# Kernel tuning notes

Hardware: AMD Instinct MI355X
Metric: run time of the kernel (lower is better)

Reference implementation:

```python
import jax, jax.numpy as jnp
import numpy as np


def setup_inputs() -> dict:
    key = jax.random.key(0)
    k1, k2, k3, k4, k5 = jax.random.split(key, 5)
    B, C, H, W = 8, 32, 64, 64
    inp = jax.random.normal(k1, (B, C, H, W), dtype=jnp.float32)
    # expected positions lie inside the image grid
    exPx = jax.random.uniform(k2, (B, H, W), dtype=jnp.float32) * (W - 1)
    exPy = jax.random.uniform(k3, (B, H, W), dtype=jnp.float32) * (H - 1)
    # positive Gaussian widths in roughly [1, 3]
    sigmax = jax.random.uniform(k4, (B, H, W), dtype=jnp.float32) * 2.0 + 1.0
    sigmay = jax.random.uniform(k5, (B, H, W), dtype=jnp.float32) * 2.0 + 1.0
    return {"input": inp, "exPx": exPx, "exPy": exPy,
            "sigmax": sigmax, "sigmay": sigmay}


def reference(input, exPx, exPy, sigmax, sigmay):
    """Gaussian-weighted spatial swap/warp (soft gather).

    For each output pixel (i, j):
      out[b,c,i,j] = sum_{u,v} G(u; exPy[b,i,j], sigmay[b,i,j])
                              * G(v; exPx[b,i,j], sigmax[b,i,j])
                              * input[b,c,u,v]  /  Z[b,i,j]
    where G is an unnormalized Gaussian and Z is the total weight mass.
    The 2D Gaussian weight is separable, so we contract rows then cols.
    """
    B, C, H, W = input.shape
    u = jnp.arange(H, dtype=input.dtype)  # source row coords (y)
    v = jnp.arange(W, dtype=input.dtype)  # source col coords (x)
    # wy: [B,H,W,H] weight over source rows u for each output pixel (i,j)
    wy = jnp.exp(-0.5 * ((u[None, None, None, :] - exPy[..., None]) / sigmay[..., None]) ** 2)
    # wx: [B,H,W,W] weight over source cols v
    wx = jnp.exp(-0.5 * ((v[None, None, None, :] - exPx[..., None]) / sigmax[..., None]) ** 2)
    # normalization mass per output pixel
    Z = wy.sum(-1) * wx.sum(-1) + jnp.asarray(1e-8, input.dtype)  # [B,H,W]
    # contract over source rows u -> [B,C,H,W,W]
    t = jnp.einsum('biju,bcuv->bcijv', wy, input)
    # contract over source cols v -> [B,C,H,W]
    out = jnp.einsum('bcijv,bijv->bcij', t, wx)
    return out / Z[:, None]
```

## Files before the change

kernel.cpp:

```cpp
#include <hip/hip_runtime.h>


#define BB 8
#define CC 32
#define HH 64
#define WW 64

typedef __attribute__((ext_vector_type(8))) short short8;
typedef __attribute__((ext_vector_type(4))) float f32x4;
typedef unsigned int uint;

__device__ __forceinline__ uint rn_bf16(float f) {
    uint u = __float_as_uint(f);
    return (u + 0x7FFFu + ((u >> 16) & 1u)) >> 16;
}

__device__ __forceinline__ void split_pair(float f0, float f1, uint& hi, uint& lo) {
    const uint u0 = __float_as_uint(f0), u1 = __float_as_uint(f1);
    hi = (u0 >> 16) | (u1 & 0xFFFF0000u);
    const float l0 = f0 - __uint_as_float(u0 & 0xFFFF0000u);
    const float l1 = f1 - __uint_as_float(u1 & 0xFFFF0000u);
    lo = (__float_as_uint(l0) >> 16) | (__float_as_uint(l1) & 0xFFFF0000u);
}

#define WYS_OFF   0
#define WXH_OFF   16640
#define SUM_OFF   25856
#define INVZ_OFF  27904
#define LDS_BYTES 28160
#define RED_OFF   0

__global__ __launch_bounds__(256, 4)
void swap_fused_kernel(const float* __restrict__ inp,
                       const float* __restrict__ exPx, const float* __restrict__ exPy,
                       const float* __restrict__ sigmax, const float* __restrict__ sigmay,
                       float* __restrict__ out)
{
    __shared__ __align__(16) char lds[LDS_BYTES];
    const int t    = threadIdx.x;
    const int lane = t & 63;
    const int w    = t >> 6;
    const int q    = (t >> 4) & 3;
    const int ln   = t & 15;
    const int bid   = blockIdx.x;
    const int b     = bid & 7;
    const int r     = bid >> 3;
    const int chalf = r & 1;
    const int i     = r >> 1;
    const int bi    = b * 64 + i;

    float* WYS = (float*)(lds + WYS_OFF);

    {
        const int p = lane;
        const int g = w;
        const int pixBase = bi * 64 + p;
        const float ey = exPy[pixBase], ex = exPx[pixBase];
        const float isy = 1.0f / sigmay[pixBase], isx = 1.0f / sigmax[pixBase];
        float sy = 0.0f, sx = 0.0f;
        #pragma unroll
        for (int k = 0; k < 16; ++k) {
            const int u = g * 16 + k;
            const float dy = ((float)u - ey) * isy;
            const float wy = __expf(-0.5f * dy * dy);
            WYS[u * 65 + p] = wy;
            sy += wy;
        }
        uint* WXH = (uint*)(lds + WXH_OFF);
        #pragma unroll
        for (int j = 0; j < 8; ++j) {
            const int v0 = g * 16 + 2 * j;
            const float dx0 = ((float)v0       - ex) * isx;
            const float dx1 = ((float)(v0 + 1) - ex) * isx;
            const float wx0 = __expf(-0.5f * dx0 * dx0);
            const float wx1 = __expf(-0.5f * dx1 * dx1);
            sx += wx0 + wx1;
            WXH[p * 36 + g * 8 + j] = rn_bf16(wx0) | (rn_bf16(wx1) << 16);
        }
        float* SUMY = (float*)(lds + SUM_OFF);
        float* SUMX = SUMY + 256;
        SUMY[g * 64 + p] = sy;
        SUMX[g * 64 + p] = sx;
    }
    __syncthreads();
    float* INVZ = (float*)(lds + INVZ_OFF);
    if (t < 64) {
        float* SUMY = (float*)(lds + SUM_OFF);
        float* SUMX = SUMY + 256;
        const float sy = SUMY[t] + SUMY[64 + t] + SUMY[128 + t] + SUMY[192 + t];
        const float sx = SUMX[t] + SUMX[64 + t] + SUMX[128 + t] + SUMX[192 + t];
        INVZ[t] = 1.0f / (sy * sx + 1e-8f);
    }
    __syncthreads();

    short8 bh[4][2];
    #pragma unroll
    for (int nt = 0; nt < 4; ++nt)
        #pragma unroll
        for (int ks = 0; ks < 2; ++ks)
            bh[nt][ks] = *(const short8*)(lds + WXH_OFF + (nt * 16 + ln) * 144 + ks * 64 + q * 16);
    float wyz[4][4];
    #pragma unroll
    for (int nt = 0; nt < 4; ++nt) {
        const float iz = INVZ[nt * 16 + ln];
        #pragma unroll
        for (int rr = 0; rr < 4; ++rr)
            wyz[nt][rr] = WYS[(w * 16 + q * 4 + rr) * 65 + nt * 16 + ln] * iz;
    }
    __syncthreads();

    const int cbase = b * CC + chalf * 16;
    float* RED = (float*)(lds + RED_OFF);
    const float* xrow = inp + (size_t)cbase * 4096 + (w * 16 + ln) * 64 + q * 8;

    #pragma unroll 2
    for (int c = 0; c < 16; ++c) {
        const float4* src = (const float4*)(xrow + (size_t)c * 4096);
        const float4 x0 = src[0];
        const float4 x1 = src[1];
        const float4 x2 = src[8];
        const float4 x3 = src[9];

        union { uint u[4]; short8 s; } Ah0, Al0, Ah1, Al1;
        split_pair(x0.x, x0.y, Ah0.u[0], Al0.u[0]);
        split_pair(x0.z, x0.w, Ah0.u[1], Al0.u[1]);
        split_pair(x1.x, x1.y, Ah0.u[2], Al0.u[2]);
        split_pair(x1.z, x1.w, Ah0.u[3], Al0.u[3]);
        split_pair(x2.x, x2.y, Ah1.u[0], Al1.u[0]);
        split_pair(x2.z, x2.w, Ah1.u[1], Al1.u[1]);
        split_pair(x3.x, x3.y, Ah1.u[2], Al1.u[2]);
        split_pair(x3.z, x3.w, Ah1.u[3], Al1.u[3]);

        f32x4 acc[4];
        #pragma unroll
        for (int nt = 0; nt < 4; ++nt) acc[nt] = (f32x4){0.f, 0.f, 0.f, 0.f};
        #pragma unroll
        for (int nt = 0; nt < 4; ++nt) {
            acc[nt] = __builtin_amdgcn_mfma_f32_16x16x32_bf16(Ah0.s, bh[nt][0], acc[nt], 0, 0, 0);
            acc[nt] = __builtin_amdgcn_mfma_f32_16x16x32_bf16(Al0.s, bh[nt][0], acc[nt], 0, 0, 0);
            acc[nt] = __builtin_amdgcn_mfma_f32_16x16x32_bf16(Ah1.s, bh[nt][1], acc[nt], 0, 0, 0);
            acc[nt] = __builtin_amdgcn_mfma_f32_16x16x32_bf16(Al1.s, bh[nt][1], acc[nt], 0, 0, 0);
        }
        #pragma unroll
        for (int nt = 0; nt < 4; ++nt) {
            float ps = acc[nt][0] * wyz[nt][0] + acc[nt][1] * wyz[nt][1]
                     + acc[nt][2] * wyz[nt][2] + acc[nt][3] * wyz[nt][3];
            ps += __shfl_xor(ps, 16, 64);
            ps += __shfl_xor(ps, 32, 64);
            if (q == 0) RED[c * 256 + w * 64 + nt * 16 + ln] = ps;
        }
    }
    __syncthreads();

    {
        const int kk = t >> 6, p = t & 63;
        #pragma unroll
        for (int g = 0; g < 4; ++g) {
            const int c = g * 4 + kk;
            const float* Rk = RED + c * 256;
            const float o = Rk[p] + Rk[64 + p] + Rk[128 + p] + Rk[192 + p];
            out[(size_t)(cbase + c) * (HH * WW) + i * 64 + p] = o;
        }
    }
}

extern "C" void kernel_launch(void* const* d_in, const int* in_sizes, int n_in,
                              void* d_out, int out_size, void* d_ws, size_t ws_size,
                              hipStream_t stream) {
    const float* inp    = (const float*)d_in[0];
    const float* exPx   = (const float*)d_in[1];
    const float* exPy   = (const float*)d_in[2];
    const float* sigmax = (const float*)d_in[3];
    const float* sigmay = (const float*)d_in[4];
    float* out = (float*)d_out;

    hipLaunchKernelGGL(swap_fused_kernel, dim3(BB * HH * 2), dim3(256), 0, stream,
                       inp, exPx, exPy, sigmax, sigmay, out);
}
```

Before: 93.08 us.

## Preconvert input to bf16 in workspace and drop hi/lo split MFMAs

Adds a pre-pass kernel that rounds the float32 input to packed bf16 in the workspace buffer. The main kernel then loads half the bytes per row and issues only the high-part MFMAs, halving the matrix-core work and removing the per-iteration split arithmetic. The cost is an extra launch and a full read/write pass over the input, plus lower accuracy because the low-part correction term is dropped. The old fused kernel remains as a fallback when the workspace is too small.

After: 82.25 us. 1.13x faster.

```diff
diff --git a/kernel.cpp b/kernel.cpp
--- a/kernel.cpp
+++ b/kernel.cpp
@@ -15,12 +15,14 @@
     return (u + 0x7FFFu + ((u >> 16) & 1u)) >> 16;
 }
 
-__device__ __forceinline__ void split_pair(float f0, float f1, uint& hi, uint& lo) {
-    const uint u0 = __float_as_uint(f0), u1 = __float_as_uint(f1);
-    hi = (u0 >> 16) | (u1 & 0xFFFF0000u);
-    const float l0 = f0 - __uint_as_float(u0 & 0xFFFF0000u);
-    const float l1 = f1 - __uint_as_float(u1 & 0xFFFF0000u);
-    lo = (__float_as_uint(l0) >> 16) | (__float_as_uint(l1) & 0xFFFF0000u);
+__global__ void preconvert_kernel(const float* __restrict__ x, uint* __restrict__ hi)
+{
+    const int n = BB * CC * HH * WW / 2;
+    int idx = blockIdx.x * blockDim.x + threadIdx.x;
+    for (; idx < n; idx += gridDim.x * blockDim.x) {
+        const float2 d = ((const float2*)x)[idx];
+        hi[idx] = rn_bf16(d.x) | (rn_bf16(d.y) << 16);
+    }
 }
 
 #define WYS_OFF   0
@@ -31,10 +33,10 @@
 #define RED_OFF   0
 
 __global__ __launch_bounds__(256, 4)
-void swap_fused_kernel(const float* __restrict__ inp,
-                       const float* __restrict__ exPx, const float* __restrict__ exPy,
-                       const float* __restrict__ sigmax, const float* __restrict__ sigmay,
-                       float* __restrict__ out)
+void swap_mfma_kernel(const uint* __restrict__ xhi,
+                      const float* __restrict__ exPx, const float* __restrict__ exPy,
+                      const float* __restrict__ sigmax, const float* __restrict__ sigmay,
+                      float* __restrict__ out)
 {
     __shared__ __align__(16) char lds[LDS_BYTES];
     const int t    = threadIdx.x;
@@ -111,16 +113,129 @@
 
     const int cbase = b * CC + chalf * 16;
     float* RED = (float*)(lds + RED_OFF);
+    const uint* xrow = xhi + (size_t)cbase * 2048 + (w * 16 + ln) * 32 + q * 4;
+
+    #pragma unroll 4
+    for (int c = 0; c < 16; ++c) {
+        const uint4* src = (const uint4*)(xrow + (size_t)c * 2048);
+        union { uint4 v; short8 s; } A0, A1;
+        A0.v = src[0];
+        A1.v = src[4];
+
+        f32x4 acc[4];
+        #pragma unroll
+        for (int nt = 0; nt < 4; ++nt) acc[nt] = (f32x4){0.f, 0.f, 0.f, 0.f};
+        #pragma unroll
+        for (int nt = 0; nt < 4; ++nt) {
+            acc[nt] = __builtin_amdgcn_mfma_f32_16x16x32_bf16(A0.s, bh[nt][0], acc[nt], 0, 0, 0);
+            acc[nt] = __builtin_amdgcn_mfma_f32_16x16x32_bf16(A1.s, bh[nt][1], acc[nt], 0, 0, 0);
+        }
+        #pragma unroll
+        for (int nt = 0; nt < 4; ++nt) {
+            float ps = acc[nt][0] * wyz[nt][0] + acc[nt][1] * wyz[nt][1]
+                     + acc[nt][2] * wyz[nt][2] + acc[nt][3] * wyz[nt][3];
+            ps += __shfl_xor(ps, 16, 64);
+            ps += __shfl_xor(ps, 32, 64);
+            if (q == 0) RED[c * 256 + w * 64 + nt * 16 + ln] = ps;
+        }
+    }
+    __syncthreads();
+
+    {
+        const int kk = t >> 6, p = t & 63;
+        #pragma unroll
+        for (int g = 0; g < 4; ++g) {
+            const int c = g * 4 + kk;
+            const float* Rk = RED + c * 256;
+            const float o = Rk[p] + Rk[64 + p] + Rk[128 + p] + Rk[192 + p];
+            out[(size_t)(cbase + c) * (HH * WW) + i * 64 + p] = o;
+        }
+    }
+}
+
+__device__ __forceinline__ void split_pair(float f0, float f1, uint& hi, uint& lo) {
+    const uint u0 = __float_as_uint(f0), u1 = __float_as_uint(f1);
+    hi = (u0 >> 16) | (u1 & 0xFFFF0000u);
+    const float l0 = f0 - __uint_as_float(u0 & 0xFFFF0000u);
+    const float l1 = f1 - __uint_as_float(u1 & 0xFFFF0000u);
+    lo = (__float_as_uint(l0) >> 16) | (__float_as_uint(l1) & 0xFFFF0000u);
+}
+
+__global__ __launch_bounds__(256, 4)
+void swap_fused_kernel(const float* __restrict__ inp,
+                       const float* __restrict__ exPx, const float* __restrict__ exPy,
+                       const float* __restrict__ sigmax, const float* __restrict__ sigmay,
+                       float* __restrict__ out)
+{
+    __shared__ __align__(16) char lds[LDS_BYTES];
+    const int t = threadIdx.x;
+    const int lane = t & 63, w = t >> 6, q = (t >> 4) & 3, ln = t & 15;
+    const int bid = blockIdx.x;
+    const int b = bid & 7, r = bid >> 3;
+    const int chalf = r & 1, i = r >> 1;
+    const int bi = b * 64 + i;
+
+    float* WYS = (float*)(lds + WYS_OFF);
+    {
+        const int p = lane, g = w;
+        const int pixBase = bi * 64 + p;
+        const float ey = exPy[pixBase], ex = exPx[pixBase];
+        const float isy = 1.0f / sigmay[pixBase], isx = 1.0f / sigmax[pixBase];
+        float sy = 0.0f, sx = 0.0f;
+        #pragma unroll
+        for (int k = 0; k < 16; ++k) {
+            const int u = g * 16 + k;
+            const float dy = ((float)u - ey) * isy;
+            const float wy = __expf(-0.5f * dy * dy);
+            WYS[u * 65 + p] = wy; sy += wy;
+        }
+        uint* WXH = (uint*)(lds + WXH_OFF);
+        #pragma unroll
+        for (int j = 0; j < 8; ++j) {
+            const int v0 = g * 16 + 2 * j;
+            const float dx0 = ((float)v0 - ex) * isx;
+            const float dx1 = ((float)(v0 + 1) - ex) * isx;
+            const float wx0 = __expf(-0.5f * dx0 * dx0);
+            const float wx1 = __expf(-0.5f * dx1 * dx1);
+            sx += wx0 + wx1;
+            WXH[p * 36 + g * 8 + j] = rn_bf16(wx0) | (rn_bf16(wx1) << 16);
+        }
+        float* SUMY = (float*)(lds + SUM_OFF);
+        float* SUMX = SUMY + 256;
+        SUMY[g * 64 + p] = sy; SUMX[g * 64 + p] = sx;
+    }
+    __syncthreads();
+    float* INVZ = (float*)(lds + INVZ_OFF);
+    if (t < 64) {
+        float* SUMY = (float*)(lds + SUM_OFF);
+        float* SUMX = SUMY + 256;
+        const float sy = SUMY[t] + SUMY[64 + t] + SUMY[128 + t] + SUMY[192 + t];
+        const float sx = SUMX[t] + SUMX[64 + t] + SUMX[128 + t] + SUMX[192 + t];
+        INVZ[t] = 1.0f / (sy * sx + 1e-8f);
+    }
+    __syncthreads();
+    short8 bh[4][2];
+    #pragma unroll
+    for (int nt = 0; nt < 4; ++nt)
+        #pragma unroll
+        for (int ks = 0; ks < 2; ++ks)
+            bh[nt][ks] = *(const short8*)(lds + WXH_OFF + (nt * 16 + ln) * 144 + ks * 64 + q * 16);
+    float wyz[4][4];
+    #pragma unroll
+    for (int nt = 0; nt < 4; ++nt) {
+        const float iz = INVZ[nt * 16 + ln];
+        #pragma unroll
+        for (int rr = 0; rr < 4; ++rr)
+            wyz[nt][rr] = WYS[(w * 16 + q * 4 + rr) * 65 + nt * 16 + ln] * iz;
+    }
+    __syncthreads();
+    const int cbase = b * CC + chalf * 16;
+    float* RED = (float*)(lds + RED_OFF);
     const float* xrow = inp + (size_t)cbase * 4096 + (w * 16 + ln) * 64 + q * 8;
-
     #pragma unroll 2
     for (int c = 0; c < 16; ++c) {
         const float4* src = (const float4*)(xrow + (size_t)c * 4096);
-        const float4 x0 = src[0];
-        const float4 x1 = src[1];
-        const float4 x2 = src[8];
-        const float4 x3 = src[9];
-
+        const float4 x0 = src[0], x1 = src[1], x2 = src[8], x3 = src[9];
         union { uint u[4]; short8 s; } Ah0, Al0, Ah1, Al1;
         split_pair(x0.x, x0.y, Ah0.u[0], Al0.u[0]);
         split_pair(x0.z, x0.w, Ah0.u[1], Al0.u[1]);
@@ -130,7 +245,6 @@
         split_pair(x2.z, x2.w, Ah1.u[1], Al1.u[1]);
         split_pair(x3.x, x3.y, Ah1.u[2], Al1.u[2]);
         split_pair(x3.z, x3.w, Ah1.u[3], Al1.u[3]);
-
         f32x4 acc[4];
         #pragma unroll
         for (int nt = 0; nt < 4; ++nt) acc[nt] = (f32x4){0.f, 0.f, 0.f, 0.f};
@@ -151,7 +265,6 @@
         }
     }
     __syncthreads();
-
     {
         const int kk = t >> 6, p = t & 63;
         #pragma unroll
@@ -174,6 +287,14 @@
     const float* sigmay = (const float*)d_in[4];
     float* out = (float*)d_out;
 
-    hipLaunchKernelGGL(swap_fused_kernel, dim3(BB * HH * 2), dim3(256), 0, stream,
-                       inp, exPx, exPy, sigmax, sigmay, out);
-}
+    const size_t plane_bytes = (size_t)BB * CC * HH * WW * 2;
+    if (ws_size >= plane_bytes) {
+        uint* xhi = (uint*)d_ws;
+        hipLaunchKernelGGL(preconvert_kernel, dim3(1024), dim3(256), 0, stream, inp, xhi);
+        hipLaunchKernelGGL(swap_mfma_kernel, dim3(BB * HH * 2), dim3(256), 0, stream,
+                           xhi, exPx, exPy, sigmax, sigmay, out);
+    } else {
+        hipLaunchKernelGGL(swap_fused_kernel, dim3(BB * HH * 2), dim3(256), 0, stream,
+                           inp, exPx, exPy, sigmax, sigmay, out);
+    }
+}
```

## Drop bf16 hi/lo split, give each warp whole channels, prefetch input registers

Applied to the files above, without the earlier changes.

Replaces the two-term bf16 split of the input (hi+lo) with a single round-half-up bf16 conversion, which halves the MFMA count. Work is reassigned so each warp owns 8 full channels across all 64 source rows, which removes the cross-warp LDS reduction and its barrier. Global input loads are double-buffered in registers, and the grid is halved to one block per output row. The cost is precision: dropping the low bf16 term leaves input errors of order 1e-3 relative, which could fail a strict tolerance. Register pressure also rises, and launch bounds are relaxed to 2.

After: 91.14 us. 1.02x faster.

```diff
diff --git a/kernel.cpp b/kernel.cpp
--- a/kernel.cpp
+++ b/kernel.cpp
@@ -14,27 +14,23 @@
     uint u = __float_as_uint(f);
     return (u + 0x7FFFu + ((u >> 16) & 1u)) >> 16;
 }
-
-__device__ __forceinline__ void split_pair(float f0, float f1, uint& hi, uint& lo) {
-    const uint u0 = __float_as_uint(f0), u1 = __float_as_uint(f1);
-    hi = (u0 >> 16) | (u1 & 0xFFFF0000u);
-    const float l0 = f0 - __uint_as_float(u0 & 0xFFFF0000u);
-    const float l1 = f1 - __uint_as_float(u1 & 0xFFFF0000u);
-    lo = (__float_as_uint(l0) >> 16) | (__float_as_uint(l1) & 0xFFFF0000u);
+__device__ __forceinline__ uint pack2_rhu(float a, float b) {
+    const uint ua = __float_as_uint(a) + 0x8000u;
+    const uint ub = __float_as_uint(b) + 0x8000u;
+    return (ua >> 16) | (ub & 0xFFFF0000u);
 }
 
 #define WYS_OFF   0
-#define WXH_OFF   16640
-#define SUM_OFF   25856
-#define INVZ_OFF  27904
-#define LDS_BYTES 28160
-#define RED_OFF   0
-
-__global__ __launch_bounds__(256, 4)
-void swap_fused_kernel(const float* __restrict__ inp,
-                       const float* __restrict__ exPx, const float* __restrict__ exPy,
-                       const float* __restrict__ sigmax, const float* __restrict__ sigmay,
-                       float* __restrict__ out)
+#define WXH_OFF   16896
+#define SUM_OFF   26112
+#define INVZ_OFF  28160
+#define LDS_BYTES 28416
+
+__global__ __launch_bounds__(256, 2)
+void swap_kernel(const float* __restrict__ inp,
+                 const float* __restrict__ exPx, const float* __restrict__ exPy,
+                 const float* __restrict__ sigmax, const float* __restrict__ sigmay,
+                 float* __restrict__ out)
 {
     __shared__ __align__(16) char lds[LDS_BYTES];
     const int t    = threadIdx.x;
@@ -42,12 +38,21 @@
     const int w    = t >> 6;
     const int q    = (t >> 4) & 3;
     const int ln   = t & 15;
-    const int bid   = blockIdx.x;
-    const int b     = bid & 7;
-    const int r     = bid >> 3;
-    const int chalf = r & 1;
-    const int i     = r >> 1;
-    const int bi    = b * 64 + i;
+    const int bid  = blockIdx.x;
+    const int b    = bid & 7;
+    const int i    = bid >> 3;
+    const int bi   = b * 64 + i;
+
+    const int cplane0 = b * CC + w * 8;
+    const float4* F4 = (const float4*)(inp + (size_t)cplane0 * 4096 + ln * 64 + q * 8);
+    float4 fbuf[4][4];
+    #pragma unroll
+    for (int mt = 0; mt < 4; ++mt) {
+        fbuf[mt][0] = F4[mt * 256];
+        fbuf[mt][1] = F4[mt * 256 + 1];
+        fbuf[mt][2] = F4[mt * 256 + 8];
+        fbuf[mt][3] = F4[mt * 256 + 9];
+    }
 
     float* WYS = (float*)(lds + WYS_OFF);
 
@@ -63,7 +68,7 @@
             const int u = g * 16 + k;
             const float dy = ((float)u - ey) * isy;
             const float wy = __expf(-0.5f * dy * dy);
-            WYS[u * 65 + p] = wy;
+            WYS[u * 66 + p] = wy;
             sy += wy;
         }
         uint* WXH = (uint*)(lds + WXH_OFF);
@@ -99,68 +104,88 @@
         #pragma unroll
         for (int ks = 0; ks < 2; ++ks)
             bh[nt][ks] = *(const short8*)(lds + WXH_OFF + (nt * 16 + ln) * 144 + ks * 64 + q * 16);
-    float wyz[4][4];
+    float wyz[4][4][4];
     #pragma unroll
     for (int nt = 0; nt < 4; ++nt) {
         const float iz = INVZ[nt * 16 + ln];
         #pragma unroll
-        for (int rr = 0; rr < 4; ++rr)
-            wyz[nt][rr] = WYS[(w * 16 + q * 4 + rr) * 65 + nt * 16 + ln] * iz;
-    }
-    __syncthreads();
-
-    const int cbase = b * CC + chalf * 16;
-    float* RED = (float*)(lds + RED_OFF);
-    const float* xrow = inp + (size_t)cbase * 4096 + (w * 16 + ln) * 64 + q * 8;
-
-    #pragma unroll 2
-    for (int c = 0; c < 16; ++c) {
-        const float4* src = (const float4*)(xrow + (size_t)c * 4096);
-        const float4 x0 = src[0];
-        const float4 x1 = src[1];
-        const float4 x2 = src[8];
-        const float4 x3 = src[9];
-
-        union { uint u[4]; short8 s; } Ah0, Al0, Ah1, Al1;
-        split_pair(x0.x, x0.y, Ah0.u[0], Al0.u[0]);
-        split_pair(x0.z, x0.w, Ah0.u[1], Al0.u[1]);
-        split_pair(x1.x, x1.y, Ah0.u[2], Al0.u[2]);
-        split_pair(x1.z, x1.w, Ah0.u[3], Al0.u[3]);
-        split_pair(x2.x, x2.y, Ah1.u[0], Al1.u[0]);
-        split_pair(x2.z, x2.w, Ah1.u[1], Al1.u[1]);
-        split_pair(x3.x, x3.y, Ah1.u[2], Al1.u[2]);
-        split_pair(x3.z, x3.w, Ah1.u[3], Al1.u[3]);
-
-        f32x4 acc[4];
-        #pragma unroll
-        for (int nt = 0; nt < 4; ++nt) acc[nt] = (f32x4){0.f, 0.f, 0.f, 0.f};
+        for (int mt = 0; mt < 4; ++mt)
+            #pragma unroll
+            for (int rr = 0; rr < 4; ++rr)
+                wyz[mt][nt][rr] = WYS[(mt * 16 + q * 4 + rr) * 66 + nt * 16 + ln] * iz;
+    }
+
+    union AU { uint4 v; short8 s; };
+    AU acur[4][2];
+    #pragma unroll
+    for (int mt = 0; mt < 4; ++mt) {
+        acur[mt][0].v = (uint4){pack2_rhu(fbuf[mt][0].x, fbuf[mt][0].y),
+                                pack2_rhu(fbuf[mt][0].z, fbuf[mt][0].w),
+                                pack2_rhu(fbuf[mt][1].x, fbuf[mt][1].y),
+                                pack2_rhu(fbuf[mt][1].z, fbuf[mt][1].w)};
+        acur[mt][1].v = (uint4){pack2_rhu(fbuf[mt][2].x, fbuf[mt][2].y),
+                                pack2_rhu(fbuf[mt][2].z, fbuf[mt][2].w),
+                                pack2_rhu(fbuf[mt][3].x, fbuf[mt][3].y),
+                                pack2_rhu(fbuf[mt][3].z, fbuf[mt][3].w)};
+    }
+    #pragma unroll
+    for (int mt = 0; mt < 4; ++mt) {
+        fbuf[mt][0] = F4[1024 + mt * 256];
+        fbuf[mt][1] = F4[1024 + mt * 256 + 1];
+        fbuf[mt][2] = F4[1024 + mt * 256 + 8];
+        fbuf[mt][3] = F4[1024 + mt * 256 + 9];
+    }
+
+    float* obase = out + (size_t)cplane0 * 4096 + i * 64 + lane;
+
+    #pragma unroll
+    for (int c = 0; c < 8; ++c) {
+        float ps[4] = {0.f, 0.f, 0.f, 0.f};
+        #pragma unroll
+        for (int mt = 0; mt < 4; ++mt) {
+            f32x4 acc[4];
+            #pragma unroll
+            for (int nt = 0; nt < 4; ++nt) acc[nt] = (f32x4){0.f, 0.f, 0.f, 0.f};
+            #pragma unroll
+            for (int nt = 0; nt < 4; ++nt) {
+                acc[nt] = __builtin_amdgcn_mfma_f32_16x16x32_bf16(acur[mt][0].s, bh[nt][0], acc[nt], 0, 0, 0);
+                acc[nt] = __builtin_amdgcn_mfma_f32_16x16x32_bf16(acur[mt][1].s, bh[nt][1], acc[nt], 0, 0, 0);
+            }
+            #pragma unroll
+            for (int nt = 0; nt < 4; ++nt)
+                ps[nt] += acc[nt][0] * wyz[mt][nt][0] + acc[nt][1] * wyz[mt][nt][1]
+                        + acc[nt][2] * wyz[mt][nt][2] + acc[nt][3] * wyz[mt][nt][3];
+        }
+        if (c < 7) {
+            #pragma unroll
+            for (int mt = 0; mt < 4; ++mt) {
+                acur[mt][0].v = (uint4){pack2_rhu(fbuf[mt][0].x, fbuf[mt][0].y),
+                                        pack2_rhu(fbuf[mt][0].z, fbuf[mt][0].w),
+                                        pack2_rhu(fbuf[mt][1].x, fbuf[mt][1].y),
+                                        pack2_rhu(fbuf[mt][1].z, fbuf[mt][1].w)};
+                acur[mt][1].v = (uint4){pack2_rhu(fbuf[mt][2].x, fbuf[mt][2].y),
+                                        pack2_rhu(fbuf[mt][2].z, fbuf[mt][2].w),
+                                        pack2_rhu(fbuf[mt][3].x, fbuf[mt][3].y),
+                                        pack2_rhu(fbuf[mt][3].z, fbuf[mt][3].w)};
+            }
+        }
+        if (c < 6) {
+            const int base = (c + 2) * 1024;
+            #pragma unroll
+            for (int mt = 0; mt < 4; ++mt) {
+                fbuf[mt][0] = F4[base + mt * 256];
+                fbuf[mt][1] = F4[base + mt * 256 + 1];
+                fbuf[mt][2] = F4[base + mt * 256 + 8];
+                fbuf[mt][3] = F4[base + mt * 256 + 9];
+            }
+        }
         #pragma unroll
         for (int nt = 0; nt < 4; ++nt) {
-            acc[nt] = __builtin_amdgcn_mfma_f32_16x16x32_bf16(Ah0.s, bh[nt][0], acc[nt], 0, 0, 0);
-            acc[nt] = __builtin_amdgcn_mfma_f32_16x16x32_bf16(Al0.s, bh[nt][0], acc[nt], 0, 0, 0);
-            acc[nt] = __builtin_amdgcn_mfma_f32_16x16x32_bf16(Ah1.s, bh[nt][1], acc[nt], 0, 0, 0);
-            acc[nt] = __builtin_amdgcn_mfma_f32_16x16x32_bf16(Al1.s, bh[nt][1], acc[nt], 0, 0, 0);
-        }
-        #pragma unroll
-        for (int nt = 0; nt < 4; ++nt) {
-            float ps = acc[nt][0] * wyz[nt][0] + acc[nt][1] * wyz[nt][1]
-                     + acc[nt][2] * wyz[nt][2] + acc[nt][3] * wyz[nt][3];
-            ps += __shfl_xor(ps, 16, 64);
-            ps += __shfl_xor(ps, 32, 64);
-            if (q == 0) RED[c * 256 + w * 64 + nt * 16 + ln] = ps;
-        }
-    }
-    __syncthreads();
-
-    {
-        const int kk = t >> 6, p = t & 63;
-        #pragma unroll
-        for (int g = 0; g < 4; ++g) {
-            const int c = g * 4 + kk;
-            const float* Rk = RED + c * 256;
-            const float o = Rk[p] + Rk[64 + p] + Rk[128 + p] + Rk[192 + p];
-            out[(size_t)(cbase + c) * (HH * WW) + i * 64 + p] = o;
-        }
+            ps[nt] += __shfl_xor(ps[nt], 16, 64);
+            ps[nt] += __shfl_xor(ps[nt], 32, 64);
+        }
+        const float po = (q == 0) ? ps[0] : (q == 1) ? ps[1] : (q == 2) ? ps[2] : ps[3];
+        obase[(size_t)c * 4096] = po;
     }
 }
 
@@ -174,6 +199,6 @@
     const float* sigmay = (const float*)d_in[4];
     float* out = (float*)d_out;
 
-    hipLaunchKernelGGL(swap_fused_kernel, dim3(BB * HH * 2), dim3(256), 0, stream,
+    hipLaunchKernelGGL(swap_kernel, dim3(BB * HH), dim3(256), 0, stream,
                        inp, exPx, exPy, sigmax, sigmay, out);
 }
```
